# Kernel tuning notes

Hardware: AMD Instinct MI355X
Metric: run time of the kernel (lower is better)

The kernel has to match this reference:

```python
import jax, jax.numpy as jnp
import numpy as np

NUM_KNOTS = 10
DEGREE = 3
N_POINTS = 8_388_608


def make_knots():
    # Mirrors BSplineBasis.__init__: clamped knot vector on [0, 1]
    inner = np.linspace(0.0, 1.0, NUM_KNOTS - 2 * DEGREE)
    return np.concatenate([np.zeros(DEGREE), inner, np.ones(DEGREE)]).astype(np.float32)


def setup_inputs() -> dict:
    key = jax.random.key(0)
    x = jax.random.normal(key, (N_POINTS,), dtype=jnp.float32)
    knots = jnp.asarray(make_knots())  # [10]
    return {"x": x, "knots": knots}


def bspline_all_bases(x, t, degree):
    """Cox-de Boor recursion evaluating ALL basis functions in one fused pass.

    x: [N] points, t: [K] knots  ->  [N, K-degree-1] basis values.
    Matches scipy BSpline.basis_element per-knot evaluation (zero outside
    support; value 1 at the clamped right endpoint for the last basis).
    """
    K = t.shape[0]
    xe = x[:, None]                       # [N, 1]
    left, right = t[None, :-1], t[None, 1:]
    # degree-0: indicator of half-open interval [t_i, t_{i+1})
    B = ((xe >= left) & (xe < right)).astype(x.dtype)   # [N, K-1]
    # include global right endpoint in the last non-degenerate interval
    B = jnp.where((xe == t[-1]) & (right == t[-1]) & (left < right),
                  jnp.asarray(1.0, x.dtype), B)
    for d in range(1, degree + 1):        # fixed small loop (degree=3)
        tL, tLd = t[: K - d - 1], t[d : K - 1]    # t_i, t_{i+d}
        tR, tRd = t[1 : K - d], t[d + 1 : K]      # t_{i+1}, t_{i+d+1}
        den1 = tLd - tL
        den2 = tRd - tR
        safe1 = jnp.where(den1 > 0, den1, 1.0)
        safe2 = jnp.where(den2 > 0, den2, 1.0)
        w1 = jnp.where(den1[None] > 0, (xe - tL[None]) / safe1[None], 0.0)
        w2 = jnp.where(den2[None] > 0, (tRd[None] - xe) / safe2[None], 0.0)
        B = w1 * B[:, :-1] + w2 * B[:, 1:]        # [N, K-1-d]
    return B                                       # [N, K-degree-1]


def reference(x, knots):
    # forward: min-max normalize to [0,1], then evaluate all B-spline bases
    x_min, x_max = x.min(), x.max()
    x_norm = (x - x_min) / (x_max - x_min + 1e-8)
    return bspline_all_bases(x_norm.ravel(), knots, DEGREE)   # [N, 6]
```

## Files before the change

### kernel.cpp

```cpp
#include <hip/hip_runtime.h>
#include <math.h>

#define NKNOTS 10
#define RED_BLOCKS 1024
#define RED_THREADS 256
#define EVAL_BLOCKS 4096
#define EVAL_THREADS 256


__device__ __forceinline__ void bspline6(float x, const float* __restrict__ t,
                                         const float* __restrict__ inv1,
                                         const float* __restrict__ inv2,
                                         const float* __restrict__ inv3,
                                         float* __restrict__ out) {
    float B[9];
    const bool at_end = (x == t[9]);
#pragma unroll
    for (int j = 0; j < 9; ++j) {
        float b = (x >= t[j] && x < t[j + 1]) ? 1.0f : 0.0f;
        if (at_end && (t[j + 1] == t[9]) && (t[j] < t[j + 1])) b = 1.0f;
        B[j] = b;
    }
#pragma unroll
    for (int j = 0; j < 8; ++j) {
        float w1 = (x - t[j]) * inv1[j];
        float w2 = (t[j + 2] - x) * inv1[j + 1];
        B[j] = w1 * B[j] + w2 * B[j + 1];
    }
#pragma unroll
    for (int j = 0; j < 7; ++j) {
        float w1 = (x - t[j]) * inv2[j];
        float w2 = (t[j + 3] - x) * inv2[j + 1];
        B[j] = w1 * B[j] + w2 * B[j + 1];
    }
#pragma unroll
    for (int j = 0; j < 6; ++j) {
        float w1 = (x - t[j]) * inv3[j];
        float w2 = (t[j + 4] - x) * inv3[j + 1];
        out[j] = w1 * B[j] + w2 * B[j + 1];
    }
}

__global__ void reduce_minmax_kernel(const float* __restrict__ x, int n,
                                     float* __restrict__ bmin,
                                     float* __restrict__ bmax) {
    float lmin = INFINITY, lmax = -INFINITY;
    int tid = blockIdx.x * blockDim.x + threadIdx.x;
    int stride = gridDim.x * blockDim.x;
    int n4 = n >> 2;
    const float4* x4 = reinterpret_cast<const float4*>(x);
    for (int i = tid; i < n4; i += stride) {
        float4 v = x4[i];
        lmin = fminf(lmin, fminf(fminf(v.x, v.y), fminf(v.z, v.w)));
        lmax = fmaxf(lmax, fmaxf(fmaxf(v.x, v.y), fmaxf(v.z, v.w)));
    }
    for (int i = (n4 << 2) + tid; i < n; i += stride) {
        float v = x[i];
        lmin = fminf(lmin, v);
        lmax = fmaxf(lmax, v);
    }
#pragma unroll
    for (int off = 32; off > 0; off >>= 1) {
        lmin = fminf(lmin, __shfl_down(lmin, off));
        lmax = fmaxf(lmax, __shfl_down(lmax, off));
    }
    __shared__ float smin[RED_THREADS / 64], smax[RED_THREADS / 64];
    int wave = threadIdx.x >> 6;
    if ((threadIdx.x & 63) == 0) { smin[wave] = lmin; smax[wave] = lmax; }
    __syncthreads();
    if (threadIdx.x == 0) {
        float m = smin[0], M = smax[0];
#pragma unroll
        for (int w = 1; w < RED_THREADS / 64; ++w) {
            m = fminf(m, smin[w]);
            M = fmaxf(M, smax[w]);
        }
        bmin[blockIdx.x] = m;
        bmax[blockIdx.x] = M;
    }
}

__global__ void finalize_kernel(const float* __restrict__ bmin,
                                const float* __restrict__ bmax, int nb,
                                const float* __restrict__ knots,
                                float* __restrict__ params) {
    float lmin = INFINITY, lmax = -INFINITY;
    for (int i = threadIdx.x; i < nb; i += blockDim.x) {
        lmin = fminf(lmin, bmin[i]);
        lmax = fmaxf(lmax, bmax[i]);
    }
#pragma unroll
    for (int off = 32; off > 0; off >>= 1) {
        lmin = fminf(lmin, __shfl_down(lmin, off));
        lmax = fmaxf(lmax, __shfl_down(lmax, off));
    }
    __shared__ float smin[4], smax[4];
    int wave = threadIdx.x >> 6;
    if ((threadIdx.x & 63) == 0) { smin[wave] = lmin; smax[wave] = lmax; }
    __syncthreads();
    if (threadIdx.x == 0) {
        float m = smin[0], M = smax[0];
#pragma unroll
        for (int w = 1; w < 4; ++w) {
            m = fminf(m, smin[w]);
            M = fmaxf(M, smax[w]);
        }
        params[0] = m;
        params[1] = M - m + 1e-8f;
        float t[NKNOTS];
#pragma unroll
        for (int j = 0; j < NKNOTS; ++j) t[j] = knots[j];
        int idx = 2;
        for (int d = 1; d <= 3; ++d) {
            for (int j = 0; j + d <= NKNOTS - 1; ++j) {
                float den = t[j + d] - t[j];
                params[idx++] = (den > 0.0f) ? (1.0f / den) : 0.0f;
            }
        }
    }
}

__global__ void eval_kernel(const float* __restrict__ x,
                            const float* __restrict__ knots,
                            const float* __restrict__ params,
                            float* __restrict__ out, int n) {
    float t[NKNOTS];
#pragma unroll
    for (int j = 0; j < NKNOTS; ++j) t[j] = knots[j];
    const float xmin = params[0];
    const float denom = params[1];
    float inv1[9], inv2[8], inv3[7];
#pragma unroll
    for (int j = 0; j < 9; ++j) inv1[j] = params[2 + j];
#pragma unroll
    for (int j = 0; j < 8; ++j) inv2[j] = params[11 + j];
#pragma unroll
    for (int j = 0; j < 7; ++j) inv3[j] = params[19 + j];

    int tid = blockIdx.x * blockDim.x + threadIdx.x;
    int stride = gridDim.x * blockDim.x;
    int npair = n >> 1;
    const float2* x2 = reinterpret_cast<const float2*>(x);
    float4* out4 = reinterpret_cast<float4*>(out);
    for (int p = tid; p < npair; p += stride) {
        float2 v = x2[p];
        float a = (v.x - xmin) / denom;
        float b = (v.y - xmin) / denom;
        float oa[6], ob[6];
        bspline6(a, t, inv1, inv2, inv3, oa);
        bspline6(b, t, inv1, inv2, inv3, ob);
        float4* o = out4 + (size_t)p * 3;
        o[0] = make_float4(oa[0], oa[1], oa[2], oa[3]);
        o[1] = make_float4(oa[4], oa[5], ob[0], ob[1]);
        o[2] = make_float4(ob[2], ob[3], ob[4], ob[5]);
    }
    if ((n & 1) && tid == 0) {
        float a = (x[n - 1] - xmin) / denom;
        float oa[6];
        bspline6(a, t, inv1, inv2, inv3, oa);
#pragma unroll
        for (int k = 0; k < 6; ++k) out[(size_t)(n - 1) * 6 + k] = oa[k];
    }
}

extern "C" void kernel_launch(void* const* d_in, const int* in_sizes, int n_in,
                              void* d_out, int out_size, void* d_ws, size_t ws_size,
                              hipStream_t stream) {
    const float* x = (const float*)d_in[0];
    const float* knots = (const float*)d_in[1];
    float* out = (float*)d_out;
    int n = in_sizes[0];

    float* wsf = (float*)d_ws;
    float* params = wsf;
    float* bmin = wsf + 32;
    float* bmax = wsf + 32 + RED_BLOCKS;

    reduce_minmax_kernel<<<RED_BLOCKS, RED_THREADS, 0, stream>>>(x, n, bmin, bmax);
    finalize_kernel<<<1, 256, 0, stream>>>(bmin, bmax, RED_BLOCKS, knots, params);
    eval_kernel<<<EVAL_BLOCKS, EVAL_THREADS, 0, stream>>>(x, knots, params, out, n);
}
```

Baseline: 253.3 us.

## Replace full Cox-de Boor recursion with span-local de Boor evaluation

Evaluates only the four nonzero cubic basis functions per point, picking the knot span from the three interior spans with two comparisons. The needed knots and reciprocal differences are precomputed once in the finalize kernel. The normalization divide becomes a multiply by a precomputed reciprocal. The eval kernel now launches one thread per four points with float4 loads instead of a grid-stride loop. This cuts per-point ALU work, but it hardcodes the 10-knot clamped layout with three active spans.

Result: slower. 344.4 us (+36.0%).

```diff
diff --git a/kernel.cpp b/kernel.cpp
--- a/kernel.cpp
+++ b/kernel.cpp
@@ -1,45 +1,10 @@
 #include <hip/hip_runtime.h>
 #include <math.h>
 
-#define NKNOTS 10
 #define RED_BLOCKS 1024
 #define RED_THREADS 256
-#define EVAL_BLOCKS 4096
 #define EVAL_THREADS 256
 
-
-__device__ __forceinline__ void bspline6(float x, const float* __restrict__ t,
-                                         const float* __restrict__ inv1,
-                                         const float* __restrict__ inv2,
-                                         const float* __restrict__ inv3,
-                                         float* __restrict__ out) {
-    float B[9];
-    const bool at_end = (x == t[9]);
-#pragma unroll
-    for (int j = 0; j < 9; ++j) {
-        float b = (x >= t[j] && x < t[j + 1]) ? 1.0f : 0.0f;
-        if (at_end && (t[j + 1] == t[9]) && (t[j] < t[j + 1])) b = 1.0f;
-        B[j] = b;
-    }
-#pragma unroll
-    for (int j = 0; j < 8; ++j) {
-        float w1 = (x - t[j]) * inv1[j];
-        float w2 = (t[j + 2] - x) * inv1[j + 1];
-        B[j] = w1 * B[j] + w2 * B[j + 1];
-    }
-#pragma unroll
-    for (int j = 0; j < 7; ++j) {
-        float w1 = (x - t[j]) * inv2[j];
-        float w2 = (t[j + 3] - x) * inv2[j + 1];
-        B[j] = w1 * B[j] + w2 * B[j + 1];
-    }
-#pragma unroll
-    for (int j = 0; j < 6; ++j) {
-        float w1 = (x - t[j]) * inv3[j];
-        float w2 = (t[j + 4] - x) * inv3[j + 1];
-        out[j] = w1 * B[j] + w2 * B[j + 1];
-    }
-}
 
 __global__ void reduce_minmax_kernel(const float* __restrict__ x, int n,
                                      float* __restrict__ bmin,
@@ -105,61 +70,106 @@
             m = fminf(m, smin[w]);
             M = fmaxf(M, smax[w]);
         }
+        float t[10];
+#pragma unroll
+        for (int j = 0; j < 10; ++j) t[j] = knots[j];
         params[0] = m;
-        params[1] = M - m + 1e-8f;
-        float t[NKNOTS];
-#pragma unroll
-        for (int j = 0; j < NKNOTS; ++j) t[j] = knots[j];
-        int idx = 2;
-        for (int d = 1; d <= 3; ++d) {
-            for (int j = 0; j + d <= NKNOTS - 1; ++j) {
-                float den = t[j + d] - t[j];
-                params[idx++] = (den > 0.0f) ? (1.0f / den) : 0.0f;
-            }
+        params[1] = 1.0f / (M - m + 1e-8f);
+        params[2] = t[4];
+        params[3] = t[5];
+        for (int kk = 0; kk < 3; ++kk) {
+            int k = 3 + kk;
+            int base = 8 + kk * 12;
+            for (int i = 0; i < 6; ++i) params[base + i] = t[k - 2 + i];
+            float d10 = t[k + 1] - t[k];
+            float d20 = t[k + 1] - t[k - 1];
+            float d21 = t[k + 2] - t[k];
+            float d30 = t[k + 1] - t[k - 2];
+            float d31 = t[k + 2] - t[k - 1];
+            float d32 = t[k + 3] - t[k];
+            params[base + 6]  = (d10 > 0.0f) ? 1.0f / d10 : 0.0f;
+            params[base + 7]  = (d20 > 0.0f) ? 1.0f / d20 : 0.0f;
+            params[base + 8]  = (d21 > 0.0f) ? 1.0f / d21 : 0.0f;
+            params[base + 9]  = (d30 > 0.0f) ? 1.0f / d30 : 0.0f;
+            params[base + 10] = (d31 > 0.0f) ? 1.0f / d31 : 0.0f;
+            params[base + 11] = (d32 > 0.0f) ? 1.0f / d32 : 0.0f;
         }
     }
 }
 
+__device__ __forceinline__ void eval6(float u, float t4, float t5,
+                                      const float W[3][12],
+                                      float* __restrict__ o) {
+    const bool c1 = (u >= t4);
+    const bool c2 = (u >= t5);
+#define SELW(i) (c2 ? W[2][i] : (c1 ? W[1][i] : W[0][i]))
+    float w0 = SELW(0), w1 = SELW(1), w2 = SELW(2);
+    float w3 = SELW(3), w4 = SELW(4), w5 = SELW(5);
+    float r10 = SELW(6), r20 = SELW(7), r21 = SELW(8);
+    float r30 = SELW(9), r31 = SELW(10), r32 = SELW(11);
+#undef SELW
+    float left1 = u - w2, left2 = u - w1, left3 = u - w0;
+    float right1 = w3 - u, right2 = w4 - u, right3 = w5 - u;
+    float temp = r10;
+    float N0 = right1 * temp;
+    float N1 = left1 * temp;
+    temp = N0 * r20;
+    N0 = right1 * temp;
+    float saved = left2 * temp;
+    temp = N1 * r21;
+    N1 = fmaf(right2, temp, saved);
+    float N2 = left1 * temp;
+    temp = N0 * r30;
+    N0 = right1 * temp;
+    saved = left3 * temp;
+    temp = N1 * r31;
+    N1 = fmaf(right2, temp, saved);
+    saved = left2 * temp;
+    temp = N2 * r32;
+    N2 = fmaf(right3, temp, saved);
+    float N3 = left1 * temp;
+    o[0] = c1 ? 0.0f : N0;
+    o[1] = c2 ? 0.0f : (c1 ? N0 : N1);
+    o[2] = c2 ? N0 : (c1 ? N1 : N2);
+    o[3] = c2 ? N1 : (c1 ? N2 : N3);
+    o[4] = c2 ? N2 : (c1 ? N3 : 0.0f);
+    o[5] = c2 ? N3 : 0.0f;
+}
+
 __global__ void eval_kernel(const float* __restrict__ x,
-                            const float* __restrict__ knots,
                             const float* __restrict__ params,
                             float* __restrict__ out, int n) {
-    float t[NKNOTS];
+    const float xmin = params[0];
+    const float invd = params[1];
+    const float t4 = params[2];
+    const float t5 = params[3];
+    float W[3][12];
 #pragma unroll
-    for (int j = 0; j < NKNOTS; ++j) t[j] = knots[j];
-    const float xmin = params[0];
-    const float denom = params[1];
-    float inv1[9], inv2[8], inv3[7];
+    for (int kk = 0; kk < 3; ++kk)
 #pragma unroll
-    for (int j = 0; j < 9; ++j) inv1[j] = params[2 + j];
+        for (int i = 0; i < 12; ++i) W[kk][i] = params[8 + kk * 12 + i];
+
+    int q = blockIdx.x * blockDim.x + threadIdx.x;
+    int nquad = n >> 2;
+    if (q < nquad) {
+        float4 v = reinterpret_cast<const float4*>(x)[q];
+        float o[24];
+        eval6((v.x - xmin) * invd, t4, t5, W, o + 0);
+        eval6((v.y - xmin) * invd, t4, t5, W, o + 6);
+        eval6((v.z - xmin) * invd, t4, t5, W, o + 12);
+        eval6((v.w - xmin) * invd, t4, t5, W, o + 18);
+        float4* o4 = reinterpret_cast<float4*>(out) + (size_t)q * 6;
 #pragma unroll
-    for (int j = 0; j < 8; ++j) inv2[j] = params[11 + j];
+        for (int s = 0; s < 6; ++s)
+            o4[s] = make_float4(o[4 * s], o[4 * s + 1], o[4 * s + 2], o[4 * s + 3]);
+    }
+    if (q == 0) {
+        for (int i = nquad << 2; i < n; ++i) {
+            float o[6];
+            eval6((x[i] - xmin) * invd, t4, t5, W, o);
 #pragma unroll
-    for (int j = 0; j < 7; ++j) inv3[j] = params[19 + j];
-
-    int tid = blockIdx.x * blockDim.x + threadIdx.x;
-    int stride = gridDim.x * blockDim.x;
-    int npair = n >> 1;
-    const float2* x2 = reinterpret_cast<const float2*>(x);
-    float4* out4 = reinterpret_cast<float4*>(out);
-    for (int p = tid; p < npair; p += stride) {
-        float2 v = x2[p];
-        float a = (v.x - xmin) / denom;
-        float b = (v.y - xmin) / denom;
-        float oa[6], ob[6];
-        bspline6(a, t, inv1, inv2, inv3, oa);
-        bspline6(b, t, inv1, inv2, inv3, ob);
-        float4* o = out4 + (size_t)p * 3;
-        o[0] = make_float4(oa[0], oa[1], oa[2], oa[3]);
-        o[1] = make_float4(oa[4], oa[5], ob[0], ob[1]);
-        o[2] = make_float4(ob[2], ob[3], ob[4], ob[5]);
-    }
-    if ((n & 1) && tid == 0) {
-        float a = (x[n - 1] - xmin) / denom;
-        float oa[6];
-        bspline6(a, t, inv1, inv2, inv3, oa);
-#pragma unroll
-        for (int k = 0; k < 6; ++k) out[(size_t)(n - 1) * 6 + k] = oa[k];
+            for (int k = 0; k < 6; ++k) out[(size_t)i * 6 + k] = o[k];
+        }
     }
 }
 
@@ -173,10 +183,13 @@
 
     float* wsf = (float*)d_ws;
     float* params = wsf;
-    float* bmin = wsf + 32;
-    float* bmax = wsf + 32 + RED_BLOCKS;
+    float* bmin = wsf + 64;
+    float* bmax = wsf + 64 + RED_BLOCKS;
 
     reduce_minmax_kernel<<<RED_BLOCKS, RED_THREADS, 0, stream>>>(x, n, bmin, bmax);
     finalize_kernel<<<1, 256, 0, stream>>>(bmin, bmax, RED_BLOCKS, knots, params);
-    eval_kernel<<<EVAL_BLOCKS, EVAL_THREADS, 0, stream>>>(x, knots, params, out, n);
+    int nquad = n >> 2;
+    int eval_blocks = (nquad + EVAL_THREADS - 1) / EVAL_THREADS;
+    if (eval_blocks < 1) eval_blocks = 1;
+    eval_kernel<<<eval_blocks, EVAL_THREADS, 0, stream>>>(x, params, out, n);
 }
```
